# Kernel tuning notes

Measured on AMD Instinct MI355X. Metric: run time of the kernel, lower is better.

Reference implementation:

```python
import jax, jax.numpy as jnp
import numpy as np

HEAD_DIM = 72
NUM_HEADS = 16
EPS = 1e-6
ROPE_THETA = 10000.0


def _rms_norm(x, scale):
    # normalize over last dim in fp32, apply learned scale
    xf = x.astype(jnp.float32)
    normed = xf * jax.lax.rsqrt(jnp.mean(xf * xf, axis=-1, keepdims=True) + EPS)
    return (normed * scale.astype(jnp.float32)).astype(x.dtype)


def _rope_cos_sin(pixel_position_ids, dtype):
    # pixel_position_ids: [B, N, 2] -> cos/sin [B, N, head_dim]
    dim = HEAD_DIM // 2                      # 36
    inv_freq = 1.0 / (ROPE_THETA ** (jnp.arange(0, dim, 2, dtype=jnp.float32) / dim))  # [18]
    pos = pixel_position_ids.astype(jnp.float32)          # [B, N, 2]
    freqs = pos[..., None] * inv_freq                      # [B, N, 2, 18]
    emb = jnp.concatenate([freqs, freqs], axis=-1)         # [B, N, 2, 36]
    cos = jnp.cos(emb)
    sin = jnp.sin(emb)
    # concat x-axis and y-axis halves -> [B, N, 72]
    cos = cos.reshape(cos.shape[0], cos.shape[1], -1)
    sin = sin.reshape(sin.shape[0], sin.shape[1], -1)
    return cos.astype(dtype), sin.astype(dtype)


def _rotate_half(x):
    half = x.shape[-1] // 2
    return jnp.concatenate([-x[..., half:], x[..., :half]], axis=-1)


def _apply_2d_rope(x, cos, sin):
    # x: [B, N, H, Dh]; cos/sin: [B, N, Dh] split into 2 spatial halves of 36 channels each
    cpd = 2 * (x.shape[-1] // 4)             # channels_per_dim = 36
    outs = []
    for k in range(2):
        xk = x[..., k * cpd:(k + 1) * cpd]
        ck = cos[:, :, None, k * cpd:(k + 1) * cpd]   # broadcast over heads (unsqueeze_dim=2)
        sk = sin[:, :, None, k * cpd:(k + 1) * cpd]
        outs.append(xk * ck + _rotate_half(xk) * sk)
    return jnp.concatenate(outs, axis=-1)


def reference(hidden_states, pixel_position_ids, Wq, Wk, Wv, Wo, q_scale, k_scale, v_scale):
    B, N, D = hidden_states.shape
    H, Dh = NUM_HEADS, HEAD_DIM
    scaling = Dh ** -0.5

    q = (hidden_states @ Wq).reshape(B, N, H, Dh)
    k = (hidden_states @ Wk).reshape(B, N, H, Dh)
    v = (hidden_states @ Wv).reshape(B, N, H, Dh)

    q = _rms_norm(q, q_scale)
    k = _rms_norm(k, k_scale)
    v = _rms_norm(v, v_scale)

    cos, sin = _rope_cos_sin(pixel_position_ids, hidden_states.dtype)
    q = _apply_2d_rope(q, cos, sin)
    k = _apply_2d_rope(k, cos, sin)

    # full softmax attention: [B, H, N, N]
    attn = jnp.einsum('bnhd,bmhd->bhnm', q, k) * scaling
    attn = jax.nn.softmax(attn, axis=-1)
    out = jnp.einsum('bhnm,bmhd->bnhd', attn, v).reshape(B, N, H * Dh)
    return out @ Wo


def setup_inputs() -> dict:
    key = jax.random.key(0)
    k1, k2, k3, k4, k5, k6 = jax.random.split(key, 6)
    B, N, D = 8, 1024, 1152
    grid = 32  # 448 / 14
    return {
        'hidden_states': jax.random.normal(k1, (B, N, D), dtype=jnp.float32),
        'pixel_position_ids': jax.random.randint(k2, (B, N, 2), 0, grid, dtype=jnp.int32),
        'Wq': jax.random.normal(k3, (D, D), dtype=jnp.float32) * 0.02,
        'Wk': jax.random.normal(k4, (D, D), dtype=jnp.float32) * 0.02,
        'Wv': jax.random.normal(k5, (D, D), dtype=jnp.float32) * 0.02,
        'Wo': jax.random.normal(k6, (D, D), dtype=jnp.float32) * 0.02,
        'q_scale': jnp.ones((HEAD_DIM,), dtype=jnp.float32),
        'k_scale': jnp.ones((HEAD_DIM,), dtype=jnp.float32),
        'v_scale': jnp.ones((HEAD_DIM,), dtype=jnp.float32),
    }
```

## Files before the change

### kernel.cpp

```cpp
#include <hip/hip_runtime.h>
#include <hip/hip_bf16.h>

typedef unsigned short u16;
typedef __attribute__((ext_vector_type(8))) short bf16x8;
typedef __attribute__((ext_vector_type(8))) unsigned short u16x8;
typedef __attribute__((ext_vector_type(4))) float f32x4;

#define NTOK 8192
#define DMODEL 1152
#define NHEAD 16
#define DHEAD 72
#define DPAD 96
#define VROWS 80
#define NQKV 3456

__device__ __forceinline__ u16 f2bf(float f){
  __hip_bfloat16 h = __float2bfloat16(f);
  return *reinterpret_cast<u16*>(&h);
}
__device__ __forceinline__ float bf2f(u16 u){
  union { unsigned int i; float f; } v; v.i = ((unsigned int)u) << 16; return v.f;
}
__device__ __forceinline__ void gload16(const void* g, void* l){
  __builtin_amdgcn_global_load_lds((const __attribute__((address_space(1))) void*)g,
                                   (__attribute__((address_space(3))) void*)l, 16, 0, 0);
}

#define FENCE asm volatile("" ::: "memory")
#define BARX() do{ FENCE; __builtin_amdgcn_s_barrier(); FENCE; }while(0)
#define LGK0 asm volatile("s_waitcnt lgkmcnt(0)" ::: "memory")
#define VMW(N) asm volatile("s_waitcnt vmcnt(" #N ")" ::: "memory")
#define PRIO1 __builtin_amdgcn_s_setprio(1)
#define PRIO0 __builtin_amdgcn_s_setprio(0)

__global__ __launch_bounds__(256) void cvt_x(const float* __restrict__ X, u16* __restrict__ Xb){
  int i = (blockIdx.x * 256 + threadIdx.x) * 8;
  float4 a = *(const float4*)(X + i);
  float4 b = *(const float4*)(X + i + 4);
  u16x8 o;
  o[0]=f2bf(a.x); o[1]=f2bf(a.y); o[2]=f2bf(a.z); o[3]=f2bf(a.w);
  o[4]=f2bf(b.x); o[5]=f2bf(b.y); o[6]=f2bf(b.z); o[7]=f2bf(b.w);
  *(u16x8*)(Xb + i) = o;
}

__global__ __launch_bounds__(256) void pack_w(const float* __restrict__ Wq, const float* __restrict__ Wk,
                                              const float* __restrict__ Wv, const float* __restrict__ Wo,
                                              u16* __restrict__ WT){
  __shared__ u16 t[32][33];
  int tx = threadIdx.x & 31, ty = threadIdx.x >> 5;
  int k0 = blockIdx.x * 32, n0 = blockIdx.y * 32;
  int ng = n0 + tx;
  const float* W; int nl;
  if (ng < 1152)      { W = Wq; nl = ng; }
  else if (ng < 2304) { W = Wk; nl = ng - 1152; }
  else if (ng < 3456) { W = Wv; nl = ng - 2304; }
  else                { W = Wo; nl = ng - 3456; }
  #pragma unroll
  for (int i = 0; i < 4; i++)
    t[ty + i*8][tx] = f2bf(W[(size_t)(k0 + ty + i*8) * 1152 + nl]);
  __syncthreads();
  #pragma unroll
  for (int i = 0; i < 4; i++)
    WT[(size_t)(n0 + ty + i*8) * 1152 + k0 + tx] = t[tx][ty + i*8];
}

__global__ __launch_bounds__(256) void rope_tab(const int* __restrict__ pid,
                                                float* __restrict__ tc, float* __restrict__ ts){
  int i = blockIdx.x * 256 + threadIdx.x;
  if (i >= NTOK * 36) return;
  int tok = i / 36, r = i - tok * 36;
  int c = r / 18, j = r - c * 18;
  float freq = exp2f(-0.7382062433f * (float)j);
  float ang = (float)pid[tok * 2 + c] * freq;
  float s, co;
  sincosf(ang, &s, &co);
  tc[i] = co; ts[i] = s;
}

#define REG(b,idx) ((b)*32768 + (idx)*8192)

__device__ __forceinline__ void stage_half(const char* g, u16* lreg, int w, int lane){
  #pragma unroll
  for (int j = 0; j < 2; j++){
    int row = j*64 + w*8 + (lane >> 3);
    int chunk = (lane & 7) ^ (row & 7);
    gload16(g + (size_t)row*2304 + chunk*16, (char*)lreg + j*8192 + w*1024);
  }
}
__device__ __forceinline__ void rdA(bf16x8 (&d)[4][2], const u16* L, int b, int wm, int mbase, int l16, int lq){
  #pragma unroll
  for (int mi = 0; mi < 4; mi++)
    #pragma unroll
    for (int kk = 0; kk < 2; kk++){
      int rl = (mbase + mi)*16 + l16;
      int byt = (rl*128 + kk*64 + lq*16) ^ ((rl & 7) << 4);
      d[mi][kk] = *(const bf16x8*)((const char*)L + (size_t)REG(b, wm)*2 + byt);
    }
}
__device__ __forceinline__ void rdB(bf16x8 (&d)[2][2], const u16* L, int b, int wn, int nbase, int l16, int lq){
  #pragma unroll
  for (int ni = 0; ni < 2; ni++)
    #pragma unroll
    for (int kk = 0; kk < 2; kk++){
      int rl = (wn & 1)*64 + (nbase + ni)*16 + l16;
      int byt = (rl*128 + kk*64 + lq*16) ^ ((rl & 7) << 4);
      d[ni][kk] = *(const bf16x8*)((const char*)L + (size_t)REG(b, 2 + (wn >> 1))*2 + byt);
    }
}
template<int MB, int NB>
__device__ __forceinline__ void quad(f32x4 (&acc)[8][4], const bf16x8 (&aa)[4][2], const bf16x8 (&bb)[2][2]){
  #pragma unroll
  for (int mi = 0; mi < 4; mi++)
    #pragma unroll
    for (int ni = 0; ni < 2; ni++)
      #pragma unroll
      for (int kk = 0; kk < 2; kk++)
        acc[MB+mi][NB+ni] = __builtin_amdgcn_mfma_f32_16x16x32_bf16(aa[mi][kk], bb[ni][kk], acc[MB+mi][NB+ni], 0, 0, 0);
}

__global__ __launch_bounds__(512, 2) void gemm256(const u16* __restrict__ A, const u16* __restrict__ Bt,
                                                  u16* __restrict__ C){
  __shared__ u16 L[65536];
  int tid = threadIdx.x, lane = tid & 63, w = tid >> 6;
  int wm = w >> 2, wn = w & 3;
  int l16 = lane & 15, lq = lane >> 4;
  int bid = blockIdx.x;
  int swz = (bid & 7) * 56 + (bid >> 3);
  int m0 = (swz & 31) * 256, n0 = (swz >> 5) * 256;
  const char* Ab = (const char*)A  + (size_t)m0 * 2304;
  const char* Bb = (const char*)Bt + (size_t)n0 * 2304;
  f32x4 acc[8][4] = {};
  bf16x8 a[4][2], a2[4][2], b0[2][2], b1[2][2];

  stage_half(Ab,                          L + REG(0,0), w, lane);
  stage_half(Ab + (size_t)128*2304,       L + REG(0,1), w, lane);
  stage_half(Bb,                          L + REG(0,2), w, lane);
  stage_half(Bb + (size_t)128*2304,       L + REG(0,3), w, lane);
  stage_half(Bb + 128,                    L + REG(1,2), w, lane);
  stage_half(Bb + (size_t)128*2304 + 128, L + REG(1,3), w, lane);
  VMW(4); BARX();

  #pragma unroll 1
  for (int i = 0; i < 9; ++i){
    bool pf = (i < 8);
    size_t k1 = (size_t)(2*i+1)*128, k2 = (size_t)(2*i+2)*128, k3 = (size_t)(2*i+3)*128;
    rdA(a,  L, 0, wm, 0, l16, lq);
    rdB(b0, L, 0, wn, 0, l16, lq);
    stage_half(Ab + k1, L + REG(1,0), w, lane);
    BARX(); LGK0; PRIO1; quad<0,0>(acc, a, b0); PRIO0; BARX();
    rdB(b1, L, 0, wn, 2, l16, lq);
    stage_half(Ab + (size_t)128*2304 + k1, L + REG(1,1), w, lane);
    BARX(); LGK0; PRIO1; quad<0,2>(acc, a, b1); PRIO0; BARX();
    rdA(a2, L, 0, wm, 4, l16, lq);
    if (pf) stage_half(Bb + k2, L + REG(0,2), w, lane);
    BARX(); LGK0; PRIO1; quad<4,0>(acc, a2, b0); PRIO0; BARX();
    if (pf) stage_half(Bb + (size_t)128*2304 + k2, L + REG(0,3), w, lane);
    BARX(); PRIO1; quad<4,2>(acc, a2, b1); PRIO0;
    if (pf) { VMW(4); } else { VMW(0); }
    BARX();
    rdA(a,  L, 1, wm, 0, l16, lq);
    rdB(b0, L, 1, wn, 0, l16, lq);
    if (pf) stage_half(Ab + k2, L + REG(0,0), w, lane);
    BARX(); LGK0; PRIO1; quad<0,0>(acc, a, b0); PRIO0; BARX();
    rdB(b1, L, 1, wn, 2, l16, lq);
    if (pf) stage_half(Ab + (size_t)128*2304 + k2, L + REG(0,1), w, lane);
    BARX(); LGK0; PRIO1; quad<0,2>(acc, a, b1); PRIO0; BARX();
    rdA(a2, L, 1, wm, 4, l16, lq);
    if (pf) stage_half(Bb + k3, L + REG(1,2), w, lane);
    BARX(); LGK0; PRIO1; quad<4,0>(acc, a2, b0); PRIO0; BARX();
    if (pf) stage_half(Bb + (size_t)128*2304 + k3, L + REG(1,3), w, lane);
    BARX(); PRIO1; quad<4,2>(acc, a2, b1); PRIO0;
    if (pf) { VMW(4); } else { VMW(0); }
    BARX();
  }
  #pragma unroll
  for (int mi = 0; mi < 8; mi++)
    #pragma unroll
    for (int ni = 0; ni < 4; ni++)
      #pragma unroll
      for (int r = 0; r < 4; r++){
        int row = m0 + wm*128 + mi*16 + lq*4 + r;
        int col = n0 + wn*64 + ni*16 + l16;
        if (col < NQKV) C[(size_t)row * NQKV + col] = f2bf(acc[mi][ni][r]);
      }
}

template<int FP32OUT>
__global__ __launch_bounds__(256) void gemm_bt(const u16* __restrict__ A, const u16* __restrict__ Bt,
                                               void* __restrict__ C, int Ncols){
  __shared__ u16 Al[128 * 64];
  __shared__ u16 Bl[128 * 64];
  int tid = threadIdx.x, lane = tid & 63, w = tid >> 6;
  int wr = w >> 1, wc = w & 1, l16 = lane & 15, lq = lane >> 4;
  int m0 = blockIdx.x * 128, n0 = blockIdx.y * 128;
  f32x4 acc[4][4] = {};
  int grow = lane >> 3;
  int gchunk = (lane & 7) ^ grow;
  const char* Abase = (const char*)A  + (size_t)(m0 + grow) * 2304 + gchunk * 16;
  const char* Bbase = (const char*)Bt + (size_t)(n0 + grow) * 2304 + gchunk * 16;
  int sw = l16 & 7;
  for (int kt = 0; kt < 18; ++kt){
    __syncthreads();
    #pragma unroll
    for (int i = 0; i < 4; i++){
      int j = w * 4 + i;
      gload16(Abase + (size_t)j * 8 * 2304 + kt * 128, &Al[j * 512]);
      gload16(Bbase + (size_t)j * 8 * 2304 + kt * 128, &Bl[j * 512]);
    }
    __syncthreads();
    #pragma unroll
    for (int kk = 0; kk < 2; kk++){
      bf16x8 af[4], bfr[4];
      #pragma unroll
      for (int m = 0; m < 4; m++){
        int row = wr * 64 + m * 16 + l16;
        af[m] = *(const bf16x8*)&Al[row * 64 + (((kk * 4 + lq) ^ sw) * 8)];
      }
      #pragma unroll
      for (int n = 0; n < 4; n++){
        int row = wc * 64 + n * 16 + l16;
        bfr[n] = *(const bf16x8*)&Bl[row * 64 + (((kk * 4 + lq) ^ sw) * 8)];
      }
      #pragma unroll
      for (int m = 0; m < 4; m++)
        #pragma unroll
        for (int n = 0; n < 4; n++)
          acc[m][n] = __builtin_amdgcn_mfma_f32_16x16x32_bf16(af[m], bfr[n], acc[m][n], 0, 0, 0);
    }
  }
  #pragma unroll
  for (int m = 0; m < 4; m++)
    #pragma unroll
    for (int n = 0; n < 4; n++)
      #pragma unroll
      for (int r = 0; r < 4; r++){
        int row = m0 + wr * 64 + m * 16 + lq * 4 + r;
        int col = n0 + wc * 64 + n * 16 + l16;
        if (FP32OUT) ((float*)C)[(size_t)row * Ncols + col] = acc[m][n][r];
        else         ((u16*)  C)[(size_t)row * Ncols + col] = f2bf(acc[m][n][r]);
      }
}

__global__ __launch_bounds__(256) void rmsrope(const u16* __restrict__ QKV,
    const float* __restrict__ tc, const float* __restrict__ ts,
    const float* __restrict__ qsc, const float* __restrict__ ksc, const float* __restrict__ vsc,
    u16* __restrict__ Qp, u16* __restrict__ Kp, u16* __restrict__ Vt){
  __shared__ u16 vl[72][264];
  int h = blockIdx.y, tid = threadIdx.x;
  int tok = blockIdx.x * 256 + tid;
  int b = tok >> 10, n = tok & 1023;
  int n0 = (blockIdx.x & 3) * 256;
  int bh = b * NHEAD + h;
  const u16* base = QKV + (size_t)tok * NQKV + h * DHEAD;

  {
    u16x8 vr[9];
    #pragma unroll
    for (int i = 0; i < 9; i++) vr[i] = *(const u16x8*)(base + 2304 + i * 8);
    float ss = 0.f;
    #pragma unroll
    for (int i = 0; i < 9; i++)
      #pragma unroll
      for (int e = 0; e < 8; e++){ float f = bf2f(vr[i][e]); ss += f * f; }
    float rv = rsqrtf(ss * (1.f / 72.f) + 1e-6f);
    #pragma unroll
    for (int i = 0; i < 9; i++)
      #pragma unroll
      for (int e = 0; e < 8; e++){
        int d = i * 8 + e;
        vl[d][tid] = f2bf(bf2f(vr[i][e]) * rv * vsc[d]);
      }
  }
  #pragma unroll
  for (int qk = 0; qk < 2; ++qk){
    const u16* src = base + qk * 1152;
    const float* sc = qk ? ksc : qsc;
    u16* dst = qk ? Kp : Qp;
    float fold = qk ? 1.0f : 0.17002219f;
    u16x8 xr[9];
    #pragma unroll
    for (int i = 0; i < 9; i++) xr[i] = *(const u16x8*)(src + i * 8);
    float ss = 0.f;
    #pragma unroll
    for (int i = 0; i < 9; i++)
      #pragma unroll
      for (int e = 0; e < 8; e++){ float f = bf2f(xr[i][e]); ss += f * f; }
    float rs_ = rsqrtf(ss * (1.f / 72.f) + 1e-6f);
    float x[72];
    #pragma unroll
    for (int i = 0; i < 9; i++)
      #pragma unroll
      for (int e = 0; e < 8; e++){ int d = i * 8 + e; x[d] = bf2f(xr[i][e]) * rs_ * sc[d]; }
    #pragma unroll
    for (int c = 0; c < 2; c++)
      #pragma unroll
      for (int j = 0; j < 18; j++){
        float co = tc[(size_t)tok * 36 + c * 18 + j];
        float si = ts[(size_t)tok * 36 + c * 18 + j];
        float x1 = x[c * 36 + j], x2 = x[c * 36 + j + 18];
        x[c * 36 + j]      = x1 * co - x2 * si;
        x[c * 36 + j + 18] = x2 * co + x1 * si;
      }
    size_t off = ((size_t)bh * 1024 + n) * DPAD;
    #pragma unroll
    for (int i = 0; i < 9; i++){
      u16x8 o;
      #pragma unroll
      for (int e = 0; e < 8; e++) o[e] = f2bf(x[i * 8 + e] * fold);
      *(u16x8*)(dst + off + i * 8) = o;
    }
    u16x8 z = {0,0,0,0,0,0,0,0};
    #pragma unroll
    for (int i = 9; i < 12; i++) *(u16x8*)(dst + off + i * 8) = z;
  }
  __syncthreads();
  u16x8 z = {0,0,0,0,0,0,0,0};
  u16x8 on = {0x3F80,0x3F80,0x3F80,0x3F80,0x3F80,0x3F80,0x3F80,0x3F80};
  for (int c = tid; c < VROWS * 32; c += 256){
    int row = c >> 5, seg = c & 31;
    u16x8 v;
    if (row < 72)       v = *(const u16x8*)&vl[row][seg * 8];
    else if (row == 72) v = on;
    else                v = z;
    *(u16x8*)(Vt + ((size_t)bh * VROWS + row) * 1024 + n0 + seg * 8) = v;
  }
}

__global__ __launch_bounds__(512, 4) void attn(const u16* __restrict__ Qp, const u16* __restrict__ Kp,
                                               const u16* __restrict__ Vt, u16* __restrict__ AO){
  __shared__ u16 Kl[64][104];
  __shared__ u16 Vl[VROWS][72];
  __shared__ u16 Pl[8][32][72];
  int tid = threadIdx.x, lane = tid & 63, w = tid >> 6;
  int l16 = lane & 15, lq = lane >> 4;
  int bh = blockIdx.y, b = bh >> 4, h = bh & 15;
  int q0 = blockIdx.x * 256;
  const u16* Qb = Qp + (size_t)bh * 1024 * DPAD;
  const u16* Kb = Kp + (size_t)bh * 1024 * DPAD;
  const u16* Vb = Vt + (size_t)bh * VROWS * 1024;

  bf16x8 qf[2][3];
  #pragma unroll
  for (int mt = 0; mt < 2; mt++)
    #pragma unroll
    for (int ks = 0; ks < 3; ks++)
      qf[mt][ks] = *(const bf16x8*)(Qb + (size_t)(q0 + w * 32 + mt * 16 + l16) * DPAD + ks * 32 + lq * 8);

  f32x4 accO[2][5] = {};

  for (int kv = 0; kv < 16; ++kv){
    __syncthreads();
    for (int c = tid; c < 768; c += 512){
      int row = c / 12, col = c - row * 12;
      *(u16x8*)&Kl[row][col * 8] = *(const u16x8*)(Kb + (size_t)(kv * 64 + row) * DPAD + col * 8);
    }
    for (int c = tid; c < VROWS * 8; c += 512){
      int row = c >> 3, seg = c & 7;
      *(u16x8*)&Vl[row][seg * 8] = *(const u16x8*)(Vb + (size_t)row * 1024 + kv * 64 + seg * 8);
    }
    __syncthreads();

    f32x4 accS[2][4] = {};
    #pragma unroll
    for (int j = 0; j < 4; j++)
      #pragma unroll
      for (int ks = 0; ks < 3; ks++){
        bf16x8 kf = *(const bf16x8*)&Kl[j * 16 + l16][ks * 32 + lq * 8];
        accS[0][j] = __builtin_amdgcn_mfma_f32_16x16x32_bf16(qf[0][ks], kf, accS[0][j], 0, 0, 0);
        accS[1][j] = __builtin_amdgcn_mfma_f32_16x16x32_bf16(qf[1][ks], kf, accS[1][j], 0, 0, 0);
      }
    #pragma unroll
    for (int mt = 0; mt < 2; mt++)
      #pragma unroll
      for (int j = 0; j < 4; j++)
        #pragma unroll
        for (int r = 0; r < 4; r++)
          Pl[w][mt * 16 + lq * 4 + r][j * 16 + l16] = f2bf(exp2f(accS[mt][j][r]));
    #pragma unroll
    for (int ks = 0; ks < 2; ks++){
      bf16x8 pf0 = *(const bf16x8*)&Pl[w][l16][ks * 32 + lq * 8];
      bf16x8 pf1 = *(const bf16x8*)&Pl[w][16 + l16][ks * 32 + lq * 8];
      #pragma unroll
      for (int nf = 0; nf < 5; nf++){
        bf16x8 vf = *(const bf16x8*)&Vl[nf * 16 + l16][ks * 32 + lq * 8];
        accO[0][nf] = __builtin_amdgcn_mfma_f32_16x16x32_bf16(pf0, vf, accO[0][nf], 0, 0, 0);
        accO[1][nf] = __builtin_amdgcn_mfma_f32_16x16x32_bf16(pf1, vf, accO[1][nf], 0, 0, 0);
      }
    }
  }
  #pragma unroll
  for (int mt = 0; mt < 2; mt++)
    #pragma unroll
    for (int r = 0; r < 4; r++){
      float s = __shfl(accO[mt][4][r], (lane & 48) + 8);
      float inv = 1.f / s;
      int qg = q0 + w * 32 + mt * 16 + lq * 4 + r;
      size_t rowoff = ((size_t)(b * 1024 + qg)) * DMODEL + h * DHEAD;
      #pragma unroll
      for (int nf = 0; nf < 5; nf++){
        int d = nf * 16 + l16;
        if (d < 72) AO[rowoff + d] = f2bf(accO[mt][nf][r] * inv);
      }
    }
}

extern "C" void kernel_launch(void* const* d_in, const int* in_sizes, int n_in,
                              void* d_out, int out_size, void* d_ws, size_t ws_size,
                              hipStream_t stream){
  const float* X   = (const float*)d_in[0];
  const int*   pid = (const int*)  d_in[1];
  const float* Wq  = (const float*)d_in[2];
  const float* Wk  = (const float*)d_in[3];
  const float* Wv  = (const float*)d_in[4];
  const float* Wo  = (const float*)d_in[5];
  const float* qsc = (const float*)d_in[6];
  const float* ksc = (const float*)d_in[7];
  const float* vsc = (const float*)d_in[8];
  char* ws = (char*)d_ws;
  u16*   Xb  = (u16*)(ws);
  u16*   WT  = (u16*)(ws + 18874368);
  u16*   QKV = (u16*)(ws + 29491200);
  u16*   Qp  = (u16*)(ws + 86114304);
  u16*   Kp  = (u16*)(ws + 111280128);
  u16*   Vt  = (u16*)(ws + 136445952);
  float* tc  = (float*)(ws + 157417472);
  float* tsn = (float*)(ws + 158597120);
  u16*   AO  = QKV;

  cvt_x  <<<4608, 256, 0, stream>>>(X, Xb);
  pack_w <<<dim3(36, 144), 256, 0, stream>>>(Wq, Wk, Wv, Wo, WT);
  rope_tab<<<1152, 256, 0, stream>>>(pid, tc, tsn);
  gemm256<<<448, 512, 0, stream>>>(Xb, WT, QKV);
  rmsrope<<<dim3(32, 16), 256, 0, stream>>>(QKV, tc, tsn, qsc, ksc, vsc, Qp, Kp, Vt);
  attn   <<<dim3(4, 128), 512, 0, stream>>>(Qp, Kp, Vt, AO);
  gemm_bt<1><<<dim3(64, 9), 256, 0, stream>>>(AO, WT + (size_t)3456 * 1152, d_out, 1152);
}
```

Baseline: 358.0 us.

## Merge prep kernels and register-prefetch next K/V tile in attention

After: 352.0 us. About the same (-1.7%).

```diff
diff --git a/kernel.cpp b/kernel.cpp
--- a/kernel.cpp
+++ b/kernel.cpp
@@ -33,48 +33,49 @@
 #define PRIO1 __builtin_amdgcn_s_setprio(1)
 #define PRIO0 __builtin_amdgcn_s_setprio(0)
 
-__global__ __launch_bounds__(256) void cvt_x(const float* __restrict__ X, u16* __restrict__ Xb){
-  int i = (blockIdx.x * 256 + threadIdx.x) * 8;
-  float4 a = *(const float4*)(X + i);
-  float4 b = *(const float4*)(X + i + 4);
-  u16x8 o;
-  o[0]=f2bf(a.x); o[1]=f2bf(a.y); o[2]=f2bf(a.z); o[3]=f2bf(a.w);
-  o[4]=f2bf(b.x); o[5]=f2bf(b.y); o[6]=f2bf(b.z); o[7]=f2bf(b.w);
-  *(u16x8*)(Xb + i) = o;
-}
-
-__global__ __launch_bounds__(256) void pack_w(const float* __restrict__ Wq, const float* __restrict__ Wk,
-                                              const float* __restrict__ Wv, const float* __restrict__ Wo,
-                                              u16* __restrict__ WT){
+__global__ __launch_bounds__(256) void prep(const float* __restrict__ X, u16* __restrict__ Xb,
+    const float* __restrict__ Wq, const float* __restrict__ Wk,
+    const float* __restrict__ Wv, const float* __restrict__ Wo, u16* __restrict__ WT,
+    const int* __restrict__ pid, float* __restrict__ tc, float* __restrict__ ts){
   __shared__ u16 t[32][33];
-  int tx = threadIdx.x & 31, ty = threadIdx.x >> 5;
-  int k0 = blockIdx.x * 32, n0 = blockIdx.y * 32;
-  int ng = n0 + tx;
-  const float* W; int nl;
-  if (ng < 1152)      { W = Wq; nl = ng; }
-  else if (ng < 2304) { W = Wk; nl = ng - 1152; }
-  else if (ng < 3456) { W = Wv; nl = ng - 2304; }
-  else                { W = Wo; nl = ng - 3456; }
-  #pragma unroll
-  for (int i = 0; i < 4; i++)
-    t[ty + i*8][tx] = f2bf(W[(size_t)(k0 + ty + i*8) * 1152 + nl]);
-  __syncthreads();
-  #pragma unroll
-  for (int i = 0; i < 4; i++)
-    WT[(size_t)(n0 + ty + i*8) * 1152 + k0 + tx] = t[tx][ty + i*8];
-}
-
-__global__ __launch_bounds__(256) void rope_tab(const int* __restrict__ pid,
-                                                float* __restrict__ tc, float* __restrict__ ts){
-  int i = blockIdx.x * 256 + threadIdx.x;
-  if (i >= NTOK * 36) return;
-  int tok = i / 36, r = i - tok * 36;
-  int c = r / 18, j = r - c * 18;
-  float freq = exp2f(-0.7382062433f * (float)j);
-  float ang = (float)pid[tok * 2 + c] * freq;
-  float s, co;
-  sincosf(ang, &s, &co);
-  tc[i] = co; ts[i] = s;
+  int bid = blockIdx.x, tid = threadIdx.x;
+  if (bid < 4608){
+    int i = (bid * 256 + tid) * 8;
+    float4 a = *(const float4*)(X + i);
+    float4 b = *(const float4*)(X + i + 4);
+    u16x8 o;
+    o[0]=f2bf(a.x); o[1]=f2bf(a.y); o[2]=f2bf(a.z); o[3]=f2bf(a.w);
+    o[4]=f2bf(b.x); o[5]=f2bf(b.y); o[6]=f2bf(b.z); o[7]=f2bf(b.w);
+    *(u16x8*)(Xb + i) = o;
+  } else if (bid < 9792){
+    int p = bid - 4608;
+    int tx = tid & 31, ty = tid >> 5;
+    int k0 = (p % 36) * 32, n0 = (p / 36) * 32;
+    int ng = n0 + tx;
+    const float* W; int nl;
+    if (ng < 1152)      { W = Wq; nl = ng; }
+    else if (ng < 2304) { W = Wk; nl = ng - 1152; }
+    else if (ng < 3456) { W = Wv; nl = ng - 2304; }
+    else                { W = Wo; nl = ng - 3456; }
+    #pragma unroll
+    for (int i = 0; i < 4; i++)
+      t[ty + i*8][tx] = f2bf(W[(size_t)(k0 + ty + i*8) * 1152 + nl]);
+    __syncthreads();
+    #pragma unroll
+    for (int i = 0; i < 4; i++)
+      WT[(size_t)(n0 + ty + i*8) * 1152 + k0 + tx] = t[tx][ty + i*8];
+  } else {
+    int i = (bid - 9792) * 256 + tid;
+    if (i < NTOK * 36){
+      int tok = i / 36, r = i - tok * 36;
+      int c = r / 18, j = r - c * 18;
+      float freq = exp2f(-0.7382062433f * (float)j);
+      float ang = (float)pid[tok * 2 + c] * freq;
+      float s, co;
+      sincosf(ang, &s, &co);
+      tc[i] = co; ts[i] = s;
+    }
+  }
 }
 
 #define REG(b,idx) ((b)*32768 + (idx)*8192)
@@ -330,7 +331,7 @@
                                                const u16* __restrict__ Vt, u16* __restrict__ AO){
   __shared__ u16 Kl[64][104];
   __shared__ u16 Vl[VROWS][72];
-  __shared__ u16 Pl[8][32][72];
+  __shared__ u16 Pl[8][32][76];
   int tid = threadIdx.x, lane = tid & 63, w = tid >> 6;
   int l16 = lane & 15, lq = lane >> 4;
   int bh = blockIdx.y, b = bh >> 4, h = bh & 15;
@@ -339,6 +340,11 @@
   const u16* Kb = Kp + (size_t)bh * 1024 * DPAD;
   const u16* Vb = Vt + (size_t)bh * VROWS * 1024;
 
+  int krow0 = tid / 12, kcol0 = tid - krow0 * 12;
+  int kc1 = tid + 512;  int krow1 = kc1 / 12, kcol1 = kc1 - krow1 * 12;
+  int vrow0 = tid >> 3, vseg0 = tid & 7;
+  int vc1 = tid + 512;  int vrow1 = vc1 >> 3, vseg1 = vc1 & 7;
+
   bf16x8 qf[2][3];
   #pragma unroll
   for (int mt = 0; mt < 2; mt++)
@@ -347,18 +353,26 @@
       qf[mt][ks] = *(const bf16x8*)(Qb + (size_t)(q0 + w * 32 + mt * 16 + l16) * DPAD + ks * 32 + lq * 8);
 
   f32x4 accO[2][5] = {};
+  u16x8 kp0, kp1, vp0, vp1;
+  kp0 = *(const u16x8*)(Kb + (size_t)krow0 * DPAD + kcol0 * 8);
+  if (tid < 256) kp1 = *(const u16x8*)(Kb + (size_t)krow1 * DPAD + kcol1 * 8);
+  vp0 = *(const u16x8*)(Vb + (size_t)vrow0 * 1024 + vseg0 * 8);
+  if (tid < 128) vp1 = *(const u16x8*)(Vb + (size_t)vrow1 * 1024 + vseg1 * 8);
 
   for (int kv = 0; kv < 16; ++kv){
-    __syncthreads();
-    for (int c = tid; c < 768; c += 512){
-      int row = c / 12, col = c - row * 12;
-      *(u16x8*)&Kl[row][col * 8] = *(const u16x8*)(Kb + (size_t)(kv * 64 + row) * DPAD + col * 8);
-    }
-    for (int c = tid; c < VROWS * 8; c += 512){
-      int row = c >> 3, seg = c & 7;
-      *(u16x8*)&Vl[row][seg * 8] = *(const u16x8*)(Vb + (size_t)row * 1024 + kv * 64 + seg * 8);
-    }
-    __syncthreads();
+    *(u16x8*)&Kl[krow0][kcol0 * 8] = kp0;
+    if (tid < 256) *(u16x8*)&Kl[krow1][kcol1 * 8] = kp1;
+    *(u16x8*)&Vl[vrow0][vseg0 * 8] = vp0;
+    if (tid < 128) *(u16x8*)&Vl[vrow1][vseg1 * 8] = vp1;
+    LGK0; BARX();
+    if (kv < 15){
+      const u16* Kn = Kb + (size_t)(kv + 1) * 64 * DPAD;
+      const u16* Vn = Vb + (size_t)(kv + 1) * 64;
+      kp0 = *(const u16x8*)(Kn + (size_t)krow0 * DPAD + kcol0 * 8);
+      if (tid < 256) kp1 = *(const u16x8*)(Kn + (size_t)krow1 * DPAD + kcol1 * 8);
+      vp0 = *(const u16x8*)(Vn + (size_t)vrow0 * 1024 + vseg0 * 8);
+      if (tid < 128) vp1 = *(const u16x8*)(Vn + (size_t)vrow1 * 1024 + vseg1 * 8);
+    }
 
     f32x4 accS[2][4] = {};
     #pragma unroll
@@ -387,6 +401,7 @@
         accO[1][nf] = __builtin_amdgcn_mfma_f32_16x16x32_bf16(pf1, vf, accO[1][nf], 0, 0, 0);
       }
     }
+    BARX();
   }
   #pragma unroll
   for (int mt = 0; mt < 2; mt++)
@@ -427,9 +442,7 @@
   float* tsn = (float*)(ws + 158597120);
   u16*   AO  = QKV;
 
-  cvt_x  <<<4608, 256, 0, stream>>>(X, Xb);
-  pack_w <<<dim3(36, 144), 256, 0, stream>>>(Wq, Wk, Wv, Wo, WT);
-  rope_tab<<<1152, 256, 0, stream>>>(pid, tc, tsn);
+  prep   <<<10944, 256, 0, stream>>>(X, Xb, Wq, Wk, Wv, Wo, WT, pid, tc, tsn);
   gemm256<<<448, 512, 0, stream>>>(Xb, WT, QKV);
   rmsrope<<<dim3(32, 16), 256, 0, stream>>>(QKV, tc, tsn, qsc, ksc, vsc, Qp, Kp, Vt);
   attn   <<<dim3(4, 128), 512, 0, stream>>>(Qp, Kp, Vt, AO);
```
